# Kernel optimization log

Measured on AMD Instinct MI355X. Metric: run time of the kernel, lower is better.

## Reference

```python
import jax, jax.numpy as jnp
import numpy as np

B, S, D = 4, 2048, 1024
N_EXPERTS, EXPERT_SIZE = 16, 256
WIDTH = N_EXPERTS * EXPERT_SIZE  # 4096


def setup_inputs() -> dict:
    key = jax.random.key(0)
    k_x, k_w1, k_w2, k_g = jax.random.split(key, 4)
    x = jax.random.normal(k_x, (B, S, D), dtype=jnp.float32)
    # Linear params, fan-in scaled init
    w1 = jax.random.normal(k_w1, (D, WIDTH), dtype=jnp.float32) / np.sqrt(D).astype(np.float32)
    b1 = jnp.zeros((WIDTH,), dtype=jnp.float32)
    w2 = jax.random.normal(k_w2, (WIDTH, D), dtype=jnp.float32) / np.sqrt(WIDTH).astype(np.float32)
    b2 = jnp.zeros((D,), dtype=jnp.float32)
    return {"x": x, "w1": w1, "b1": b1, "w2": w2, "b2": b2}


def reference(x, w1, b1, w2, b2):
    # NOTE: the original module computes expert-choice routing tensors
    # (gate einsum -> topk -> one_hot -> identity matmul 'gather'), but the
    # returned value is ONLY the dense FFN applied to x; all routing results
    # are dead code with no effect on the output. Faithful output math:
    h = jax.nn.relu(jnp.einsum('bsd,dw->bsw', x, w1) + b1)  # [B,S,WIDTH]
    return jnp.einsum('bsw,wd->bsd', h, w2) + b2            # [B,S,D]
```

## Files before the change

### kernel.cpp

```cpp
#include <hip/hip_runtime.h>
#include <hip/hip_bf16.h>


typedef __bf16 bf16;
typedef __bf16 bf16x4 __attribute__((ext_vector_type(4)));
typedef __bf16 bf16x8 __attribute__((ext_vector_type(8)));
typedef float  f32x4  __attribute__((ext_vector_type(4)));

#define BM 128
#define BN 128
#define BK 32

__device__ __forceinline__ void gload_lds16(const bf16* g, bf16* l) {
    __builtin_amdgcn_global_load_lds(
        (const __attribute__((address_space(1))) unsigned int*)g,
        (__attribute__((address_space(3))) unsigned int*)l,
        16, 0, 0);
}

__global__ __launch_bounds__(256) void cast_f32_bf16(
    const float4* __restrict__ in, bf16x4* __restrict__ out, int n4)
{
    int i = blockIdx.x * 256 + threadIdx.x;
    if (i < n4) {
        float4 v = in[i];
        bf16x4 o;
        o.x = (bf16)v.x; o.y = (bf16)v.y; o.z = (bf16)v.z; o.w = (bf16)v.w;
        out[i] = o;
    }
}

__global__ __launch_bounds__(256) void transpose_cast(
    const float* __restrict__ in, bf16* __restrict__ out, int K, int N)
{
    __shared__ __align__(16) bf16 tile[64][72];
    const int k0 = blockIdx.y * 64;
    const int n0 = blockIdx.x * 64;
    const int t  = threadIdx.x;

    const int lr = t >> 4;
    const int lc = (t & 15) << 2;
#pragma unroll
    for (int p = 0; p < 4; ++p) {
        int k = p * 16 + lr;
        float4 v = *(const float4*)(in + (size_t)(k0 + k) * N + n0 + lc);
        tile[lc + 0][k] = (bf16)v.x;
        tile[lc + 1][k] = (bf16)v.y;
        tile[lc + 2][k] = (bf16)v.z;
        tile[lc + 3][k] = (bf16)v.w;
    }
    __syncthreads();

    const int wr = t >> 3;
    const int wc = (t & 7) << 3;
#pragma unroll
    for (int p = 0; p < 2; ++p) {
        int n = p * 32 + wr;
        *(bf16x8*)(out + (size_t)(n0 + n) * K + k0 + wc) =
            *(const bf16x8*)&tile[n][wc];
    }
}

template <int FUSE_RELU_BF16>
__global__ __launch_bounds__(256) void gemm_bt(
    const bf16* __restrict__ A, const bf16* __restrict__ Bt,
    const float* __restrict__ bias, void* __restrict__ Cout,
    int M, int N, int K)
{
    __shared__ __align__(16) bf16 As[BM * BK];
    __shared__ __align__(16) bf16 Bs[BN * BK];

    const int tid  = threadIdx.x;
    const int wave = tid >> 6;
    const int lane = tid & 63;

    const int sr = lane >> 2;
    const int sc = (lane & 3) << 3;
    const size_t K_ = (size_t)K;

    const bf16* ga0 = A  + ((size_t)blockIdx.y * BM + wave * 16 + sr) * K_ + sc;
    const bf16* gb0 = Bt + ((size_t)blockIdx.x * BN + wave * 16 + sr) * K_ + sc;
    const bf16* ga1 = ga0 + 64 * K_;
    const bf16* gb1 = gb0 + 64 * K_;

    bf16* la0 = &As[(wave * 16 + sr) * BK + sc];
    bf16* la1 = la0 + 64 * BK;
    bf16* lb0 = &Bs[(wave * 16 + sr) * BK + sc];
    bf16* lb1 = lb0 + 64 * BK;

    const int wm   = (wave >> 1) << 6;
    const int wn   = (wave & 1) << 6;
    const int quad = lane >> 4;
    const int r    = lane & 15;

    f32x4 acc[4][4] = {};

    for (int k0 = 0; k0 < K; k0 += BK) {
        __syncthreads();
        gload_lds16(ga0, la0);
        gload_lds16(ga1, la1);
        gload_lds16(gb0, lb0);
        gload_lds16(gb1, lb1);
        ga0 += BK; ga1 += BK; gb0 += BK; gb1 += BK;
        __syncthreads();

        bf16x8 af[4], bfr[4];
#pragma unroll
        for (int i = 0; i < 4; ++i)
            af[i] = *(const bf16x8*)&As[(wm + i * 16 + r) * BK + (quad << 3)];
#pragma unroll
        for (int j = 0; j < 4; ++j)
            bfr[j] = *(const bf16x8*)&Bs[(wn + j * 16 + r) * BK + (quad << 3)];
#pragma unroll
        for (int i = 0; i < 4; ++i)
#pragma unroll
            for (int j = 0; j < 4; ++j)
                acc[i][j] = __builtin_amdgcn_mfma_f32_16x16x32_bf16(
                    af[i], bfr[j], acc[i][j], 0, 0, 0);
    }

    const int m_base = blockIdx.y * BM + wm + quad * 4;
    const int n_base = blockIdx.x * BN + wn + r;
    float bv[4];
#pragma unroll
    for (int j = 0; j < 4; ++j) bv[j] = bias[n_base + j * 16];

    if (FUSE_RELU_BF16) {
        bf16* Cb = (bf16*)Cout;
#pragma unroll
        for (int i = 0; i < 4; ++i) {
#pragma unroll
            for (int p = 0; p < 4; ++p) {
                size_t row = (size_t)(m_base + i * 16 + p) * (size_t)N;
#pragma unroll
                for (int j = 0; j < 4; ++j) {
                    float v = acc[i][j][p] + bv[j];
                    v = v > 0.f ? v : 0.f;
                    Cb[row + n_base + j * 16] = (bf16)v;
                }
            }
        }
    } else {
        float* Cf = (float*)Cout;
#pragma unroll
        for (int i = 0; i < 4; ++i) {
#pragma unroll
            for (int p = 0; p < 4; ++p) {
                size_t row = (size_t)(m_base + i * 16 + p) * (size_t)N;
#pragma unroll
                for (int j = 0; j < 4; ++j) {
                    Cf[row + n_base + j * 16] = acc[i][j][p] + bv[j];
                }
            }
        }
    }
}

extern "C" void kernel_launch(void* const* d_in, const int* in_sizes, int n_in,
                              void* d_out, int out_size, void* d_ws, size_t ws_size,
                              hipStream_t stream)
{
    const float* x  = (const float*)d_in[0];
    const float* w1 = (const float*)d_in[1];
    const float* b1 = (const float*)d_in[2];
    const float* w2 = (const float*)d_in[3];
    const float* b2 = (const float*)d_in[4];
    float* out = (float*)d_out;

    const int M = 8192, D = 1024, W = 4096;

    char* ws = (char*)d_ws;
    bf16* xb  = (bf16*)(ws);
    bf16* w1t = (bf16*)(ws + (size_t)(16 << 20));
    bf16* w2t = (bf16*)(ws + (size_t)(24 << 20));
    bf16* h   = (bf16*)(ws + (size_t)(32 << 20));

    {
        int n4 = (M * D) / 4;
        cast_f32_bf16<<<(n4 + 255) / 256, 256, 0, stream>>>(
            (const float4*)x, (bf16x4*)xb, n4);
    }
    transpose_cast<<<dim3(W / 64, D / 64), 256, 0, stream>>>(w1, w1t, D, W);
    transpose_cast<<<dim3(D / 64, W / 64), 256, 0, stream>>>(w2, w2t, W, D);

    gemm_bt<1><<<dim3(W / BN, M / BM), 256, 0, stream>>>(
        xb, w1t, b1, (void*)h, M, W, D);

    gemm_bt<0><<<dim3(D / BN, M / BM), 256, 0, stream>>>(
        h, w2t, b2, (void*)out, M, D, W);
}
```

Baseline: 309.4 us.

## Double K tile to 64 with XOR-swizzled LDS layout and occupancy hint

Raises the K tile from 32 to 64 so each barrier pair covers twice as many MFMAs, which halves the synchronization count per output tile. The LDS layout gets an XOR swizzle on the 16-byte chunk index to avoid bank conflicts on the wider rows. Global loads are remapped so each wave loads 8 rows of 128 bytes per instruction. A launch-bounds minimum of 3 blocks per CU is added, which doubles LDS use per block and may constrain registers.

```diff
diff --git a/kernel.cpp b/kernel.cpp
--- a/kernel.cpp
+++ b/kernel.cpp
@@ -9,7 +9,7 @@
 
 #define BM 128
 #define BN 128
-#define BK 32
+#define BK 64
 
 __device__ __forceinline__ void gload_lds16(const bf16* g, bf16* l) {
     __builtin_amdgcn_global_load_lds(
@@ -62,7 +62,7 @@
 }
 
 template <int FUSE_RELU_BF16>
-__global__ __launch_bounds__(256) void gemm_bt(
+__global__ __launch_bounds__(256, 3) void gemm_bt(
     const bf16* __restrict__ A, const bf16* __restrict__ Bt,
     const float* __restrict__ bias, void* __restrict__ Cout,
     int M, int N, int K)
@@ -74,49 +74,57 @@
     const int wave = tid >> 6;
     const int lane = tid & 63;
 
-    const int sr = lane >> 2;
-    const int sc = (lane & 3) << 3;
+    const int l8  = lane >> 3;
+    const int c8  = lane & 7;
+    const int swc = (c8 ^ l8) << 3;
     const size_t K_ = (size_t)K;
 
-    const bf16* ga0 = A  + ((size_t)blockIdx.y * BM + wave * 16 + sr) * K_ + sc;
-    const bf16* gb0 = Bt + ((size_t)blockIdx.x * BN + wave * 16 + sr) * K_ + sc;
-    const bf16* ga1 = ga0 + 64 * K_;
-    const bf16* gb1 = gb0 + 64 * K_;
-
-    bf16* la0 = &As[(wave * 16 + sr) * BK + sc];
-    bf16* la1 = la0 + 64 * BK;
-    bf16* lb0 = &Bs[(wave * 16 + sr) * BK + sc];
-    bf16* lb1 = lb0 + 64 * BK;
+    const bf16* gA[4]; const bf16* gB[4];
+    bf16* lA[4]; bf16* lB[4];
+#pragma unroll
+    for (int g = 0; g < 4; ++g) {
+        const int rr = wave * 32 + g * 8 + l8;
+        gA[g] = A  + ((size_t)blockIdx.y * BM + rr) * K_ + swc;
+        gB[g] = Bt + ((size_t)blockIdx.x * BN + rr) * K_ + swc;
+        lA[g] = &As[(wave * 32 + g * 8) * BK] + lane * 8;
+        lB[g] = &Bs[(wave * 32 + g * 8) * BK] + lane * 8;
+    }
 
     const int wm   = (wave >> 1) << 6;
     const int wn   = (wave & 1) << 6;
     const int quad = lane >> 4;
     const int r    = lane & 15;
+    const int r7   = lane & 7;
 
     f32x4 acc[4][4] = {};
 
     for (int k0 = 0; k0 < K; k0 += BK) {
         __syncthreads();
-        gload_lds16(ga0, la0);
-        gload_lds16(ga1, la1);
-        gload_lds16(gb0, lb0);
-        gload_lds16(gb1, lb1);
-        ga0 += BK; ga1 += BK; gb0 += BK; gb1 += BK;
+#pragma unroll
+        for (int g = 0; g < 4; ++g) {
+            gload_lds16(gA[g], lA[g]);
+            gload_lds16(gB[g], lB[g]);
+            gA[g] += BK; gB[g] += BK;
+        }
         __syncthreads();
 
-        bf16x8 af[4], bfr[4];
 #pragma unroll
-        for (int i = 0; i < 4; ++i)
-            af[i] = *(const bf16x8*)&As[(wm + i * 16 + r) * BK + (quad << 3)];
+        for (int h = 0; h < 2; ++h) {
+            const int ch = ((h * 4 + quad) ^ r7) << 3;
+            bf16x8 af[4], bfr[4];
 #pragma unroll
-        for (int j = 0; j < 4; ++j)
-            bfr[j] = *(const bf16x8*)&Bs[(wn + j * 16 + r) * BK + (quad << 3)];
-#pragma unroll
-        for (int i = 0; i < 4; ++i)
+            for (int i = 0; i < 4; ++i)
+                af[i] = *(const bf16x8*)&As[(wm + i * 16 + r) * BK + ch];
 #pragma unroll
             for (int j = 0; j < 4; ++j)
-                acc[i][j] = __builtin_amdgcn_mfma_f32_16x16x32_bf16(
-                    af[i], bfr[j], acc[i][j], 0, 0, 0);
+                bfr[j] = *(const bf16x8*)&Bs[(wn + j * 16 + r) * BK + ch];
+#pragma unroll
+            for (int i = 0; i < 4; ++i)
+#pragma unroll
+                for (int j = 0; j < 4; ++j)
+                    acc[i][j] = __builtin_amdgcn_mfma_f32_16x16x32_bf16(
+                        af[i], bfr[j], acc[i][j], 0, 0, 0);
+        }
     }
 
     const int m_base = blockIdx.y * BM + wm + quad * 4;
```

After: 252.5 us. 18.4% less time.
